# Kernel optimization log

Measured on AMD Instinct MI355X. Metric: run time of the kernel, lower is better.

Reference implementation:

```python
import jax, jax.numpy as jnp
import numpy as np
from jax import lax

B, N, C = 2, 4160, 512
HID = 2048
NUM_HEADS = 4
HEAD_DIM = C // NUM_HEADS
LN_EPS = 1e-5


def setup_inputs() -> dict:
    key = jax.random.key(0)
    ks = jax.random.split(key, 16)
    std = 0.02
    inp = {
        "x": jax.random.normal(ks[0], (B, N, C), dtype=jnp.float32),
        "ln1_w": jnp.ones((C,), jnp.float32), "ln1_b": jnp.zeros((C,), jnp.float32),
        "ln2_w": jnp.ones((C,), jnp.float32), "ln2_b": jnp.zeros((C,), jnp.float32),
        "q_w": jax.random.normal(ks[1], (C, C), jnp.float32) * std,
        "q_b": jnp.zeros((C,), jnp.float32),
        "kv_w": jax.random.normal(ks[2], (2 * C, C), jnp.float32) * std,
        "kv_b": jnp.zeros((2 * C,), jnp.float32),
        "proj_w": jax.random.normal(ks[3], (C, C), jnp.float32) * std,
        "proj_b": jnp.zeros((C,), jnp.float32),
        "fc1_w": jax.random.normal(ks[4], (HID, C), jnp.float32) * std,
        "fc1_b": jnp.zeros((HID,), jnp.float32),
        "dw_w": jax.random.normal(ks[5], (HID, 1, 3), jnp.float32) * np.sqrt(2.0 / 3.0),
        "dw_b": jnp.zeros((HID,), jnp.float32),
        "fc2_w": jax.random.normal(ks[6], (C, HID), jnp.float32) * std,
        "fc2_b": jnp.zeros((C,), jnp.float32),
        "px1_w": jax.random.normal(ks[7], (2 * C, C), jnp.float32) * std,
        "px1_b": jnp.zeros((2 * C,), jnp.float32),
        "px2_w": jax.random.normal(ks[8], (C, 2 * C), jnp.float32) * std,
        "px2_b": jnp.zeros((C,), jnp.float32),
        "gamma1": jnp.full((C,), 1e-6, jnp.float32),
        "gamma2": jnp.full((C,), 1e-6, jnp.float32),
        "H": 4096,
        "semantic_len": 64,
    }
    return inp


def _ln(x, w, b):
    mu = jnp.mean(x, axis=-1, keepdims=True)
    var = jnp.mean(jnp.square(x - mu), axis=-1, keepdims=True)
    return (x - mu) * lax.rsqrt(var + LN_EPS) * w + b


def _linear(x, w, b):
    return jnp.einsum('...i,oi->...o', x, w) + b


def _attention(x, q_w, q_b, kv_w, kv_b, proj_w, proj_b):
    b, n, c = x.shape
    h, d = NUM_HEADS, HEAD_DIM
    q = _linear(x, q_w, q_b).reshape(b, n, h, d).transpose(0, 2, 1, 3)   # bhnd
    kv = _linear(x, kv_w, kv_b).reshape(b, n, 2, h, d).transpose(2, 0, 3, 1, 4)
    k, v = kv[0], kv[1]                                                   # bhnd
    scale = d ** -0.5
    attn = jax.nn.softmax(jnp.einsum('bhnd,bhmd->bhnm', q, k) * scale, axis=-1)
    out = jnp.einsum('bhnm,bhmd->bhnd', attn, v).transpose(0, 2, 1, 3).reshape(b, n, c)
    return _linear(out, proj_w, proj_b)


def _dwconv(x, w, b):
    # x: [B, H, HID] -> conv over token axis, depthwise
    xt = x.transpose(0, 2, 1)  # NCH
    y = lax.conv_general_dilated(xt, w, window_strides=(1,), padding=((1, 1),),
                                 feature_group_count=HID,
                                 dimension_numbers=('NCH', 'OIH', 'NCH'))
    return (y + b[None, :, None]).transpose(0, 2, 1)


def _merge_ffn(x, H, fc1_w, fc1_b, dw_w, dw_b, fc2_w, fc2_b, px1_w, px1_b, px2_w, px2_b):
    seq = x[:, :H, :]
    sem = x[:, H:, :]
    sem = _linear(jax.nn.gelu(_linear(sem, px1_w, px1_b), approximate=False), px2_w, px2_b)
    seq = _linear(seq, fc1_w, fc1_b)
    seq = jax.nn.gelu(_dwconv(seq, dw_w, dw_b), approximate=False)
    seq = _linear(seq, fc2_w, fc2_b)
    return jnp.concatenate([seq, sem], axis=1)


def reference(x, ln1_w, ln1_b, ln2_w, ln2_b, q_w, q_b, kv_w, kv_b, proj_w, proj_b,
              fc1_w, fc1_b, dw_w, dw_b, fc2_w, fc2_b, px1_w, px1_b, px2_w, px2_b,
              gamma1, gamma2, H, semantic_len):
    x = x + gamma1 * _attention(_ln(x, ln1_w, ln1_b), q_w, q_b, kv_w, kv_b, proj_w, proj_b)
    x = x + gamma2 * _merge_ffn(_ln(x, ln2_w, ln2_b), H,
                                fc1_w, fc1_b, dw_w, dw_b, fc2_w, fc2_b,
                                px1_w, px1_b, px2_w, px2_b)
    return x
```

## Files before the change

### kernel.cpp

```cpp
#include <hip/hip_runtime.h>
#include <stdint.h>

#define BB 2
#define NN 4160
#define CC 512
#define HIDD 2048
#define HH 4096
#define QSCALE 0.12751742f
#define KSPLIT 6
#define KTILES 11

typedef short bf16x8 __attribute__((ext_vector_type(8)));
typedef float f32x4 __attribute__((ext_vector_type(4)));
typedef float f32x16 __attribute__((ext_vector_type(16)));

__device__ __forceinline__ float bf2f(ushort u){
  union { uint32_t u32; float f; } c; c.u32 = ((uint32_t)u) << 16; return c.f;
}
__device__ __forceinline__ ushort f2bf(float f){
  union { float f; uint32_t u32; } c; c.f = f;
  uint32_t r = c.u32 + 0x7fffu + ((c.u32 >> 16) & 1u);
  return (ushort)(r >> 16);
}
__device__ __forceinline__ float gelu_f(float x){
  return 0.5f * x * (1.0f + erff(x * 0.70710678118654752440f));
}
__device__ __forceinline__ void async16(ushort* lds, const ushort* g){
  __builtin_amdgcn_global_load_lds(
      (const __attribute__((address_space(1))) uint32_t*)g,
      (__attribute__((address_space(3))) uint32_t*)lds, 16, 0, 0);
}
__device__ __forceinline__ uint32_t cvtpk_bf16(float a, float b){
  uint32_t r;
  asm("v_cvt_pk_bf16_f32 %0, %1, %2" : "=v"(r) : "v"(a), "v"(b));
  return r;
}
__device__ __forceinline__ void swap32(uint32_t& x, uint32_t& y){
  asm("v_permlane32_swap_b32 %0, %1" : "+v"(x), "+v"(y));
}

template<int MODE>
__device__ __forceinline__ int rowmap(int m){
  if (MODE == 0) return m;
  if (MODE == 1) return (m >> 12) * NN + (m & 4095);
  return (m >> 6) * NN + HH + (m & 63);
}

__global__ __launch_bounds__(256) void wconv_kernel(
    const float* __restrict__ s0, const float* __restrict__ s1,
    const float* __restrict__ s2, const float* __restrict__ s3,
    const float* __restrict__ s4, const float* __restrict__ s5,
    const float* __restrict__ s6, ushort* __restrict__ dst)
{
  int i4 = (blockIdx.x * 256 + threadIdx.x) * 4;
  const float* s; int off;
  if      (i4 <  262144){ s = s0; off = 0;       }
  else if (i4 <  786432){ s = s1; off = 262144;  }
  else if (i4 < 1048576){ s = s2; off = 786432;  }
  else if (i4 < 2097152){ s = s3; off = 1048576; }
  else if (i4 < 3145728){ s = s4; off = 2097152; }
  else if (i4 < 3670016){ s = s5; off = 3145728; }
  else                  { s = s6; off = 3670016; }
  float4 v = *(const float4*)(s + (i4 - off));
  union { ushort h[4]; uint2 u; } o;
  o.h[0] = f2bf(v.x); o.h[1] = f2bf(v.y); o.h[2] = f2bf(v.z); o.h[3] = f2bf(v.w);
  *(uint2*)(dst + i4) = o.u;
}

__global__ __launch_bounds__(256) void ln_kernel(
    const float* __restrict__ x, const float* __restrict__ w,
    const float* __restrict__ b, ushort* __restrict__ out)
{
  int row  = blockIdx.x * 4 + (threadIdx.x >> 6);
  int lane = threadIdx.x & 63;
  const float4* xr = (const float4*)(x + (size_t)row * CC);
  float4 v0 = xr[lane];
  float4 v1 = xr[lane + 64];
  float s  = v0.x + v0.y + v0.z + v0.w + v1.x + v1.y + v1.z + v1.w;
  float ss = v0.x*v0.x + v0.y*v0.y + v0.z*v0.z + v0.w*v0.w
           + v1.x*v1.x + v1.y*v1.y + v1.z*v1.z + v1.w*v1.w;
  #pragma unroll
  for (int off = 1; off < 64; off <<= 1){
    s  += __shfl_xor(s, off);
    ss += __shfl_xor(ss, off);
  }
  float mu  = s * (1.0f / CC);
  float var = ss * (1.0f / CC) - mu * mu;
  float rs  = rsqrtf(var + 1e-5f);
  const float4* wp = (const float4*)w;
  const float4* bp = (const float4*)b;
  float4 w0 = wp[lane], w1 = wp[lane + 64], b0 = bp[lane], b1 = bp[lane + 64];
  union { ushort h[4]; uint2 u; } o0, o1;
  o0.h[0] = f2bf((v0.x - mu) * rs * w0.x + b0.x);
  o0.h[1] = f2bf((v0.y - mu) * rs * w0.y + b0.y);
  o0.h[2] = f2bf((v0.z - mu) * rs * w0.z + b0.z);
  o0.h[3] = f2bf((v0.w - mu) * rs * w0.w + b0.w);
  o1.h[0] = f2bf((v1.x - mu) * rs * w1.x + b1.x);
  o1.h[1] = f2bf((v1.y - mu) * rs * w1.y + b1.y);
  o1.h[2] = f2bf((v1.z - mu) * rs * w1.z + b1.z);
  o1.h[3] = f2bf((v1.w - mu) * rs * w1.w + b1.w);
  ushort* orow = out + (size_t)row * CC;
  ((uint2*)orow)[lane]      = o0.u;
  ((uint2*)orow)[lane + 64] = o1.u;
}

template<int BN, int AMAP, int OMAP, int EPI>
__global__ __launch_bounds__(256) void gemm_kernel(
    const ushort* __restrict__ A, int lda,
    const ushort* __restrict__ W,
    const float* __restrict__ bias, const float* __restrict__ bias2,
    ushort* __restrict__ outb, ushort* __restrict__ outb2,
    float* __restrict__ outf,
    const float* __restrict__ resid, const float* __restrict__ gamma,
    ushort* __restrict__ vt, int K, int O)
{
  constexpr int NCT = BN / 32;
  __shared__ __align__(16) ushort As[128 * 64];
  __shared__ __align__(16) ushort Ws[BN * 64];
  int tid  = threadIdx.x;
  int lane = tid & 63;
  int wv   = tid >> 6;
  int w0   = wv & 1, w1 = wv >> 1;
  int quad = lane >> 4, l16 = lane & 15;
  int m0 = blockIdx.x * 128;
  int o0 = blockIdx.y * BN;

  f32x4 acc[4][NCT];
  f32x4 zf = {0.f, 0.f, 0.f, 0.f};
  #pragma unroll
  for (int i = 0; i < 4; i++)
    #pragma unroll
    for (int j = 0; j < NCT; j++) acc[i][j] = zf;

  for (int k0 = 0; k0 < K; k0 += 64){
    __syncthreads();
    #pragma unroll
    for (int i = 0; i < 4; i++){
      int o = i * 256 + tid;
      int row = o >> 3, c = (o & 7) ^ (row & 7);
      int gm = rowmap<AMAP>(m0 + row);
      async16(&As[o * 8], A + (size_t)gm * lda + k0 + c * 8);
    }
    #pragma unroll
    for (int i = 0; i < BN * 8 / 256; i++){
      int o = i * 256 + tid;
      int row = o >> 3, c = (o & 7) ^ (row & 7);
      async16(&Ws[o * 8], W + (size_t)(o0 + row) * K + k0 + c * 8);
    }
    __syncthreads();
    #pragma unroll
    for (int kk = 0; kk < 2; kk++){
      bf16x8 af[4], bfr[NCT];
      #pragma unroll
      for (int rt = 0; rt < 4; rt++){
        int row = w1 * 64 + rt * 16 + l16;
        af[rt] = *(const bf16x8*)&As[(row * 8 + ((kk * 4 + quad) ^ (row & 7))) * 8];
      }
      #pragma unroll
      for (int ct = 0; ct < NCT; ct++){
        int row = w0 * (BN / 2) + ct * 16 + l16;
        bfr[ct] = *(const bf16x8*)&Ws[(row * 8 + ((kk * 4 + quad) ^ (row & 7))) * 8];
      }
      #pragma unroll
      for (int rt = 0; rt < 4; rt++)
        #pragma unroll
        for (int ct = 0; ct < NCT; ct++)
          acc[rt][ct] = __builtin_amdgcn_mfma_f32_16x16x32_bf16(af[rt], bfr[ct], acc[rt][ct], 0, 0, 0);
    }
  }

  #pragma unroll
  for (int ct = 0; ct < NCT; ct++){
    int col = o0 + w0 * (BN / 2) + ct * 16 + l16;
    #pragma unroll
    for (int rt = 0; rt < 4; rt++){
      int mb = m0 + w1 * 64 + rt * 16 + quad * 4;
      if (EPI == 3){
        if (col < 512){
          float bs = bias[col];
          #pragma unroll
          for (int r = 0; r < 4; r++)
            outb[(size_t)(mb + r) * 512 + col] = f2bf((acc[rt][ct][r] + bs) * QSCALE);
        } else if (col < 1024){
          float bs = bias2[col - 512];
          #pragma unroll
          for (int r = 0; r < 4; r++)
            outb2[(size_t)(mb + r) * 512 + (col - 512)] = f2bf(acc[rt][ct][r] + bs);
        } else {
          float bs = bias2[col - 512];
          int dd = col - 1024;
          int h2 = dd >> 7, d = dd & 127;
          int bbat = (mb >= NN) ? 1 : 0;
          int n = mb - bbat * NN;
          union { ushort h[4]; uint2 u; } pk;
          #pragma unroll
          for (int r = 0; r < 4; r++) pk.h[r] = f2bf(acc[rt][ct][r] + bs);
          *(uint2*)&vt[((size_t)((bbat * 4 + h2) * 128 + d)) * NN + n] = pk.u;
        }
      } else {
        float bs = bias[col];
        #pragma unroll
        for (int r = 0; r < 4; r++){
          float v = acc[rt][ct][r] + bs;
          if (EPI == 1) v = gelu_f(v);
          if (EPI == 0 || EPI == 1){
            outb[(size_t)rowmap<OMAP>(mb + r) * O + col] = f2bf(v);
          } else {
            size_t off = (size_t)rowmap<OMAP>(mb + r) * O + col;
            outf[off] = resid[off] + gamma[col] * v;
          }
        }
      }
    }
  }
}

__global__ __launch_bounds__(256, 2) void attn_kernel(
    const ushort* __restrict__ q, const ushort* __restrict__ kbuf,
    const ushort* __restrict__ vt, ushort* __restrict__ opart, float* __restrict__ ml)
{
  __shared__ __align__(16) ushort Ks[2][64 * 128];
  __shared__ __align__(16) ushort VTs[2][128 * 64];
  __shared__ float Als[4][32];
  int tid = threadIdx.x, lane = tid & 63, wv = tid >> 6;
  int l31 = lane & 31, hf = lane >> 5;
  int qt = blockIdx.x, bh = blockIdx.y, ks = blockIdx.z;
  int b = bh >> 2, h = bh & 3;
  int jt0 = ks * KTILES;
  int jt1 = jt0 + KTILES; if (jt1 > 65) jt1 = 65;

  const ushort* kg0 = kbuf + ((size_t)b * NN) * CC + h * 128;
  const ushort* vg0 = vt + ((size_t)bh * 128) * NN;

  auto stage = [&](int bsel, int t){
    const ushort* kgb = kg0 + (size_t)(t * 64) * CC;
    const ushort* vgb = vg0 + t * 64;
    #pragma unroll
    for (int i = 0; i < 4; i++){
      int oo = i * 256 + tid;
      int row = oo >> 4, ck = (oo & 15) ^ (row & 7);
      async16(&Ks[bsel][oo * 8], kgb + (size_t)row * CC + ck * 8);
      int d = oo >> 3, cv = (oo & 7) ^ (d & 7);
      async16(&VTs[bsel][oo * 8], vgb + (size_t)d * NN + cv * 8);
    }
  };

  stage(0, jt0);

  int qr = qt * 128 + wv * 32 + l31;
  qr = (qr < NN) ? qr : (NN - 1);
  const ushort* qrow = q + ((size_t)(b * NN + qr)) * CC + h * 128 + hf * 8;
  bf16x8 qf[8];
  #pragma unroll
  for (int kk = 0; kk < 8; kk++)
    qf[kk] = *(const bf16x8*)(qrow + kk * 16);

  float mrow = -1e30f, lrow = 0.f;
  f32x16 o[4];
  #pragma unroll
  for (int dt = 0; dt < 4; dt++)
    #pragma unroll
    for (int r = 0; r < 16; r++) o[dt][r] = 0.f;

  int cur = 0;
  for (int jt = jt0; jt < jt1; jt++){
    __syncthreads();
    if (jt + 1 < jt1) stage(cur ^ 1, jt + 1);
    const ushort* Kb = Ks[cur];
    const ushort* Vb = VTs[cur];

    f32x16 s0, s1;
    #pragma unroll
    for (int r = 0; r < 16; r++){ s0[r] = 0.f; s1[r] = 0.f; }
    __builtin_amdgcn_s_setprio(1);
    #pragma unroll
    for (int kk = 0; kk < 8; kk++){
      int r0 = l31, r1 = 32 + l31;
      bf16x8 kf0 = *(const bf16x8*)&Kb[(r0 * 16 + ((kk * 2 + hf) ^ (r0 & 7))) * 8];
      bf16x8 kf1 = *(const bf16x8*)&Kb[(r1 * 16 + ((kk * 2 + hf) ^ (r1 & 7))) * 8];
      s0 = __builtin_amdgcn_mfma_f32_32x32x16_bf16(kf0, qf[kk], s0, 0, 0, 0);
      s1 = __builtin_amdgcn_mfma_f32_32x32x16_bf16(kf1, qf[kk], s1, 0, 0, 0);
    }
    __builtin_amdgcn_s_setprio(0);

    float mx = s0[0];
    #pragma unroll
    for (int r = 1; r < 16; r++) mx = fmaxf(mx, s0[r]);
    #pragma unroll
    for (int r = 0; r < 16; r++) mx = fmaxf(mx, s1[r]);
    mx = fmaxf(mx, __shfl_xor(mx, 32));

    if (__any(mx > mrow + 8.0f)){
      float mn = fmaxf(mrow, mx);
      float al = __builtin_amdgcn_exp2f(mrow - mn);
      mrow = mn;
      lrow *= al;
      if (lane < 32) Als[wv][l31] = al;
      #pragma unroll
      for (int g = 0; g < 4; g++){
        float4 ag = *(const float4*)&Als[wv][8 * g + 4 * hf];
        float agr[4] = {ag.x, ag.y, ag.z, ag.w};
        #pragma unroll
        for (int dt = 0; dt < 4; dt++)
          #pragma unroll
          for (int r = 0; r < 4; r++)
            o[dt][4 * g + r] *= agr[r];
      }
    }

    float t = 0.f;
    #pragma unroll
    for (int r = 0; r < 16; r++){ s0[r] = __builtin_amdgcn_exp2f(s0[r] - mrow); t += s0[r]; }
    #pragma unroll
    for (int r = 0; r < 16; r++){ s1[r] = __builtin_amdgcn_exp2f(s1[r] - mrow); t += s1[r]; }
    t += __shfl_xor(t, 32);
    lrow += t;

    union PU { uint32_t w[4]; bf16x8 v; };
    bf16x8 pa[4];
    {
      uint32_t Aw = cvtpk_bf16(s0[0],  s0[1]);
      uint32_t Bw = cvtpk_bf16(s0[2],  s0[3]);
      uint32_t Cw = cvtpk_bf16(s0[4],  s0[5]);
      uint32_t Dw = cvtpk_bf16(s0[6],  s0[7]);
      swap32(Aw, Cw); swap32(Bw, Dw);
      PU u0; u0.w[0] = Aw; u0.w[1] = Bw; u0.w[2] = Cw; u0.w[3] = Dw; pa[0] = u0.v;
      uint32_t Ew = cvtpk_bf16(s0[8],  s0[9]);
      uint32_t Fw = cvtpk_bf16(s0[10], s0[11]);
      uint32_t Gw = cvtpk_bf16(s0[12], s0[13]);
      uint32_t Hw = cvtpk_bf16(s0[14], s0[15]);
      swap32(Ew, Gw); swap32(Fw, Hw);
      PU u1; u1.w[0] = Ew; u1.w[1] = Fw; u1.w[2] = Gw; u1.w[3] = Hw; pa[1] = u1.v;
      uint32_t Iw = cvtpk_bf16(s1[0],  s1[1]);
      uint32_t Jw = cvtpk_bf16(s1[2],  s1[3]);
      uint32_t Kw = cvtpk_bf16(s1[4],  s1[5]);
      uint32_t Lw = cvtpk_bf16(s1[6],  s1[7]);
      swap32(Iw, Kw); swap32(Jw, Lw);
      PU u2; u2.w[0] = Iw; u2.w[1] = Jw; u2.w[2] = Kw; u2.w[3] = Lw; pa[2] = u2.v;
      uint32_t Mw = cvtpk_bf16(s1[8],  s1[9]);
      uint32_t Nw = cvtpk_bf16(s1[10], s1[11]);
      uint32_t Ow = cvtpk_bf16(s1[12], s1[13]);
      uint32_t Pw = cvtpk_bf16(s1[14], s1[15]);
      swap32(Mw, Ow); swap32(Nw, Pw);
      PU u3; u3.w[0] = Mw; u3.w[1] = Nw; u3.w[2] = Ow; u3.w[3] = Pw; pa[3] = u3.v;
    }

    __builtin_amdgcn_s_setprio(1);
    #pragma unroll
    for (int k4 = 0; k4 < 4; k4++)
      #pragma unroll
      for (int dt = 0; dt < 4; dt++){
        int d = dt * 32 + l31;
        bf16x8 vf = *(const bf16x8*)&Vb[(d * 8 + ((k4 * 2 + hf) ^ (d & 7))) * 8];
        o[dt] = __builtin_amdgcn_mfma_f32_32x32x16_bf16(pa[k4], vf, o[dt], 0, 0, 0);
      }
    __builtin_amdgcn_s_setprio(0);
    cur ^= 1;
  }

  int part = (qt * 8 + bh) * KSPLIT + ks;
  if (lane < 32){
    ml[(size_t)part * 256 + wv * 32 + l31]       = mrow;
    ml[(size_t)part * 256 + 128 + wv * 32 + l31] = lrow;
  }
  ushort* op = opart + (size_t)part * 16384;
  #pragma unroll
  for (int g = 0; g < 4; g++)
    #pragma unroll
    for (int dt = 0; dt < 4; dt++){
      uint2 pk;
      pk.x = cvtpk_bf16(o[dt][4 * g + 0], o[dt][4 * g + 1]);
      pk.y = cvtpk_bf16(o[dt][4 * g + 2], o[dt][4 * g + 3]);
      *(uint2*)&op[((((wv * 4 + g) * 4 + dt) * 64) + lane) * 4] = pk;
    }
}

__global__ __launch_bounds__(256) void attn_combine_kernel(
    const ushort* __restrict__ opart, const float* __restrict__ ml,
    ushort* __restrict__ out)
{
  int qt = blockIdx.x, bh = blockIdx.y;
  int b = bh >> 2, hd = bh & 3;
  int tid = threadIdx.x, lane = tid & 63, wq = tid >> 6;
  int l31 = lane & 31, hf = lane >> 5;
  int base = (qt * 8 + bh) * KSPLIT;

  #pragma unroll
  for (int g = 0; g < 4; g++){
    int qb = wq * 32 + 8 * g + 4 * hf;
    float mv[KSPLIT][4], lv[KSPLIT][4];
    #pragma unroll
    for (int p = 0; p < KSPLIT; p++){
      float4 m = *(const float4*)&ml[(size_t)(base + p) * 256 + qb];
      float4 l = *(const float4*)&ml[(size_t)(base + p) * 256 + 128 + qb];
      mv[p][0] = m.x; mv[p][1] = m.y; mv[p][2] = m.z; mv[p][3] = m.w;
      lv[p][0] = l.x; lv[p][1] = l.y; lv[p][2] = l.z; lv[p][3] = l.w;
    }
    float wr[KSPLIT][4], invr[4];
    #pragma unroll
    for (int r = 0; r < 4; r++){
      float mx = mv[0][r];
      #pragma unroll
      for (int p = 1; p < KSPLIT; p++) mx = fmaxf(mx, mv[p][r]);
      float den = 0.f;
      #pragma unroll
      for (int p = 0; p < KSPLIT; p++){
        wr[p][r] = __builtin_amdgcn_exp2f(mv[p][r] - mx);
        den += wr[p][r] * lv[p][r];
      }
      invr[r] = 1.0f / den;
    }
    #pragma unroll
    for (int dt = 0; dt < 4; dt++){
      int idx = (((wq * 4 + g) * 4 + dt) * 64 + lane) * 4;
      float acc[4] = {0.f, 0.f, 0.f, 0.f};
      #pragma unroll
      for (int p = 0; p < KSPLIT; p++){
        union { ushort h[4]; uint2 u; } a;
        a.u = *(const uint2*)&opart[(size_t)(base + p) * 16384 + idx];
        #pragma unroll
        for (int r = 0; r < 4; r++) acc[r] += wr[p][r] * bf2f(a.h[r]);
      }
      #pragma unroll
      for (int r = 0; r < 4; r++){
        int n = qt * 128 + qb + r;
        if (n < NN)
          out[((size_t)(b * NN + n)) * CC + hd * 128 + dt * 32 + l31] = f2bf(acc[r] * invr[r]);
      }
    }
  }
}

__global__ __launch_bounds__(256) void dwconv_kernel(
    const ushort* __restrict__ u, const float* __restrict__ w,
    const float* __restrict__ bia, ushort* __restrict__ out)
{
  int g = blockIdx.x * 256 + threadIdx.x;
  int row = g >> 8;
  int c8 = (g & 255) * 8;
  int n = row & (HH - 1);
  size_t base = (size_t)row * HIDD + c8;
  uint4 z4; z4.x = z4.y = z4.z = z4.w = 0;
  uint4 u1 = *(const uint4*)(u + base);
  uint4 u0 = (n > 0)      ? *(const uint4*)(u + base - HIDD) : z4;
  uint4 u2 = (n < HH - 1) ? *(const uint4*)(u + base + HIDD) : z4;
  const ushort* p0 = (const ushort*)&u0;
  const ushort* p1 = (const ushort*)&u1;
  const ushort* p2 = (const ushort*)&u2;
  union { ushort h[8]; uint4 v; } o;
  #pragma unroll
  for (int k = 0; k < 8; k++){
    int c = c8 + k;
    float acc = bia[c] + w[c * 3] * bf2f(p0[k]) + w[c * 3 + 1] * bf2f(p1[k]) + w[c * 3 + 2] * bf2f(p2[k]);
    o.h[k] = f2bf(gelu_f(acc));
  }
  *(uint4*)(out + base) = o.v;
}

extern "C" void kernel_launch(void* const* d_in, const int* in_sizes, int n_in,
                              void* d_out, int out_size, void* d_ws, size_t ws_size,
                              hipStream_t stream)
{
  const float* x      = (const float*)d_in[0];
  const float* ln1w   = (const float*)d_in[1];
  const float* ln1b   = (const float*)d_in[2];
  const float* ln2w   = (const float*)d_in[3];
  const float* ln2b   = (const float*)d_in[4];
  const float* q_b    = (const float*)d_in[6];
  const float* kv_b   = (const float*)d_in[8];
  const float* proj_b = (const float*)d_in[10];
  const float* fc1_b  = (const float*)d_in[12];
  const float* dw_w   = (const float*)d_in[13];
  const float* dw_b   = (const float*)d_in[14];
  const float* fc2_b  = (const float*)d_in[16];
  const float* px1_b  = (const float*)d_in[18];
  const float* px2_b  = (const float*)d_in[20];
  const float* gamma1 = (const float*)d_in[21];
  const float* gamma2 = (const float*)d_in[22];
  float* out = (float*)d_out;

  char* ws = (char*)d_ws;
  ushort* wbf = (ushort*)(ws);
  ushort* lnb = (ushort*)(ws + 8388608);
  ushort* qb  = (ushort*)(ws + 16908288);
  ushort* kb  = (ushort*)(ws + 25427968);
  ushort* vtb = (ushort*)(ws + 33947648);
  ushort* ab  = (ushort*)(ws + 42467328);
  ushort* opart = (ushort*)(ws + 50987008);
  float*  mlb   = (float*)(ws + 102891520);
  ushort* f1  = (ushort*)(ws + 50987008);
  ushort* dg  = (ushort*)(ws + 84541440);
  ushort* sm1 = (ushort*)(ws + 118095872);

  ushort* wq    = wbf;
  ushort* wproj = wbf + 786432;
  ushort* wfc1  = wbf + 1048576;
  ushort* wfc2  = wbf + 2097152;
  ushort* wpx1  = wbf + 3145728;
  ushort* wpx2  = wbf + 3670016;

  wconv_kernel<<<4096, 256, 0, stream>>>((const float*)d_in[5], (const float*)d_in[7],
                                         (const float*)d_in[9], (const float*)d_in[11],
                                         (const float*)d_in[15], (const float*)d_in[17],
                                         (const float*)d_in[19], wbf);
  ln_kernel<<<2080, 256, 0, stream>>>(x, ln1w, ln1b, lnb);
  gemm_kernel<128,0,0,3><<<dim3(65, 12), 256, 0, stream>>>(
      lnb, 512, wq, q_b, kv_b, qb, kb, nullptr, nullptr, nullptr, vtb, 512, 1536);
  attn_kernel<<<dim3(33, 8, KSPLIT), 256, 0, stream>>>(qb, kb, vtb, opart, mlb);
  attn_combine_kernel<<<dim3(33, 8), 256, 0, stream>>>(opart, mlb, ab);
  gemm_kernel<64,0,0,2><<<dim3(65, 8), 256, 0, stream>>>(
      ab, 512, wproj, proj_b, nullptr, nullptr, nullptr, out, x, gamma1, nullptr, 512, 512);
  ln_kernel<<<2080, 256, 0, stream>>>(out, ln2w, ln2b, lnb);
  gemm_kernel<128,1,0,0><<<dim3(64, 16), 256, 0, stream>>>(
      lnb, 512, wfc1, fc1_b, nullptr, f1, nullptr, nullptr, nullptr, nullptr, nullptr, 512, 2048);
  dwconv_kernel<<<8192, 256, 0, stream>>>(f1, dw_w, dw_b, dg);
  gemm_kernel<64,0,1,2><<<dim3(64, 8), 256, 0, stream>>>(
      dg, 2048, wfc2, fc2_b, nullptr, nullptr, nullptr, out, out, gamma2, nullptr, 2048, 512);
  gemm_kernel<64,2,0,1><<<dim3(1, 16), 256, 0, stream>>>(
      lnb, 512, wpx1, px1_b, nullptr, sm1, nullptr, nullptr, nullptr, nullptr, nullptr, 512, 1024);
  gemm_kernel<64,0,2,2><<<dim3(1, 8), 256, 0, stream>>>(
      sm1, 1024, wpx2, px2_b, nullptr, nullptr, nullptr, out, out, gamma2, nullptr, 1024, 512);
}
```

Before: 461.4 us.

## Halve attention KV tile to 32 rows and raise occupancy to four blocks

```diff
diff --git a/kernel.cpp b/kernel.cpp
--- a/kernel.cpp
+++ b/kernel.cpp
@@ -7,8 +7,9 @@
 #define HIDD 2048
 #define HH 4096
 #define QSCALE 0.12751742f
-#define KSPLIT 6
-#define KTILES 11
+#define KSPLIT 7
+#define KTILES 19
+#define NKT 130
 
 typedef short bf16x8 __attribute__((ext_vector_type(8)));
 typedef float f32x4 __attribute__((ext_vector_type(4)));
@@ -215,32 +216,32 @@
   }
 }
 
-__global__ __launch_bounds__(256, 2) void attn_kernel(
+__global__ __launch_bounds__(256, 4) void attn_kernel(
     const ushort* __restrict__ q, const ushort* __restrict__ kbuf,
     const ushort* __restrict__ vt, ushort* __restrict__ opart, float* __restrict__ ml)
 {
-  __shared__ __align__(16) ushort Ks[2][64 * 128];
-  __shared__ __align__(16) ushort VTs[2][128 * 64];
+  __shared__ __align__(16) ushort Ks[2][32 * 128];
+  __shared__ __align__(16) ushort VTs[2][128 * 32];
   __shared__ float Als[4][32];
   int tid = threadIdx.x, lane = tid & 63, wv = tid >> 6;
   int l31 = lane & 31, hf = lane >> 5;
   int qt = blockIdx.x, bh = blockIdx.y, ks = blockIdx.z;
   int b = bh >> 2, h = bh & 3;
   int jt0 = ks * KTILES;
-  int jt1 = jt0 + KTILES; if (jt1 > 65) jt1 = 65;
+  int jt1 = jt0 + KTILES; if (jt1 > NKT) jt1 = NKT;
 
   const ushort* kg0 = kbuf + ((size_t)b * NN) * CC + h * 128;
   const ushort* vg0 = vt + ((size_t)bh * 128) * NN;
 
   auto stage = [&](int bsel, int t){
-    const ushort* kgb = kg0 + (size_t)(t * 64) * CC;
-    const ushort* vgb = vg0 + t * 64;
-    #pragma unroll
-    for (int i = 0; i < 4; i++){
+    const ushort* kgb = kg0 + (size_t)(t * 32) * CC;
+    const ushort* vgb = vg0 + t * 32;
+    #pragma unroll
+    for (int i = 0; i < 2; i++){
       int oo = i * 256 + tid;
       int row = oo >> 4, ck = (oo & 15) ^ (row & 7);
       async16(&Ks[bsel][oo * 8], kgb + (size_t)row * CC + ck * 8);
-      int d = oo >> 3, cv = (oo & 7) ^ (d & 7);
+      int d = oo >> 2, cv = (oo & 3) ^ (d & 3);
       async16(&VTs[bsel][oo * 8], vgb + (size_t)d * NN + cv * 8);
     }
   };
@@ -269,25 +270,23 @@
     const ushort* Kb = Ks[cur];
     const ushort* Vb = VTs[cur];
 
-    f32x16 s0, s1;
-    #pragma unroll
-    for (int r = 0; r < 16; r++){ s0[r] = 0.f; s1[r] = 0.f; }
+    f32x16 s0;
+    #pragma unroll
+    for (int r = 0; r < 16; r++) s0[r] = 0.f;
     __builtin_amdgcn_s_setprio(1);
     #pragma unroll
     for (int kk = 0; kk < 8; kk++){
-      int r0 = l31, r1 = 32 + l31;
+      int r0 = l31;
       bf16x8 kf0 = *(const bf16x8*)&Kb[(r0 * 16 + ((kk * 2 + hf) ^ (r0 & 7))) * 8];
-      bf16x8 kf1 = *(const bf16x8*)&Kb[(r1 * 16 + ((kk * 2 + hf) ^ (r1 & 7))) * 8];
       s0 = __builtin_amdgcn_mfma_f32_32x32x16_bf16(kf0, qf[kk], s0, 0, 0, 0);
-      s1 = __builtin_amdgcn_mfma_f32_32x32x16_bf16(kf1, qf[kk], s1, 0, 0, 0);
     }
     __builtin_amdgcn_s_setprio(0);
 
-    float mx = s0[0];
-    #pragma unroll
-    for (int r = 1; r < 16; r++) mx = fmaxf(mx, s0[r]);
-    #pragma unroll
-    for (int r = 0; r < 16; r++) mx = fmaxf(mx, s1[r]);
+    float mx = fmaxf(
+        fmaxf(fmaxf(fmaxf(s0[0], s0[1]),  fmaxf(s0[2],  s0[3])),
+              fmaxf(fmaxf(s0[4], s0[5]),  fmaxf(s0[6],  s0[7]))),
+        fmaxf(fmaxf(fmaxf(s0[8], s0[9]),  fmaxf(s0[10], s0[11])),
+              fmaxf(fmaxf(s0[12], s0[13]), fmaxf(s0[14], s0[15]))));
     mx = fmaxf(mx, __shfl_xor(mx, 32));
 
     if (__any(mx > mrow + 8.0f)){
@@ -308,21 +307,20 @@
       }
     }
 
-    float t = 0.f;
-    #pragma unroll
-    for (int r = 0; r < 16; r++){ s0[r] = __builtin_amdgcn_exp2f(s0[r] - mrow); t += s0[r]; }
-    #pragma unroll
-    for (int r = 0; r < 16; r++){ s1[r] = __builtin_amdgcn_exp2f(s1[r] - mrow); t += s1[r]; }
+    #pragma unroll
+    for (int r = 0; r < 16; r++) s0[r] = __builtin_amdgcn_exp2f(s0[r] - mrow);
+    float t = (((s0[0] + s0[1]) + (s0[2] + s0[3])) + ((s0[4] + s0[5]) + (s0[6] + s0[7])))
+            + (((s0[8] + s0[9]) + (s0[10] + s0[11])) + ((s0[12] + s0[13]) + (s0[14] + s0[15])));
     t += __shfl_xor(t, 32);
     lrow += t;
 
     union PU { uint32_t w[4]; bf16x8 v; };
-    bf16x8 pa[4];
+    bf16x8 pa[2];
     {
-      uint32_t Aw = cvtpk_bf16(s0[0],  s0[1]);
-      uint32_t Bw = cvtpk_bf16(s0[2],  s0[3]);
-      uint32_t Cw = cvtpk_bf16(s0[4],  s0[5]);
-      uint32_t Dw = cvtpk_bf16(s0[6],  s0[7]);
+      uint32_t Aw = cvtpk_bf16(s0[0], s0[1]);
+      uint32_t Bw = cvtpk_bf16(s0[2], s0[3]);
+      uint32_t Cw = cvtpk_bf16(s0[4], s0[5]);
+      uint32_t Dw = cvtpk_bf16(s0[6], s0[7]);
       swap32(Aw, Cw); swap32(Bw, Dw);
       PU u0; u0.w[0] = Aw; u0.w[1] = Bw; u0.w[2] = Cw; u0.w[3] = Dw; pa[0] = u0.v;
       uint32_t Ew = cvtpk_bf16(s0[8],  s0[9]);
@@ -331,27 +329,15 @@
       uint32_t Hw = cvtpk_bf16(s0[14], s0[15]);
       swap32(Ew, Gw); swap32(Fw, Hw);
       PU u1; u1.w[0] = Ew; u1.w[1] = Fw; u1.w[2] = Gw; u1.w[3] = Hw; pa[1] = u1.v;
-      uint32_t Iw = cvtpk_bf16(s1[0],  s1[1]);
-      uint32_t Jw = cvtpk_bf16(s1[2],  s1[3]);
-      uint32_t Kw = cvtpk_bf16(s1[4],  s1[5]);
-      uint32_t Lw = cvtpk_bf16(s1[6],  s1[7]);
-      swap32(Iw, Kw); swap32(Jw, Lw);
-      PU u2; u2.w[0] = Iw; u2.w[1] = Jw; u2.w[2] = Kw; u2.w[3] = Lw; pa[2] = u2.v;
-      uint32_t Mw = cvtpk_bf16(s1[8],  s1[9]);
-      uint32_t Nw = cvtpk_bf16(s1[10], s1[11]);
-      uint32_t Ow = cvtpk_bf16(s1[12], s1[13]);
-      uint32_t Pw = cvtpk_bf16(s1[14], s1[15]);
-      swap32(Mw, Ow); swap32(Nw, Pw);
-      PU u3; u3.w[0] = Mw; u3.w[1] = Nw; u3.w[2] = Ow; u3.w[3] = Pw; pa[3] = u3.v;
     }
 
     __builtin_amdgcn_s_setprio(1);
     #pragma unroll
-    for (int k4 = 0; k4 < 4; k4++)
+    for (int k4 = 0; k4 < 2; k4++)
       #pragma unroll
       for (int dt = 0; dt < 4; dt++){
         int d = dt * 32 + l31;
-        bf16x8 vf = *(const bf16x8*)&Vb[(d * 8 + ((k4 * 2 + hf) ^ (d & 7))) * 8];
+        bf16x8 vf = *(const bf16x8*)&Vb[(d * 4 + ((k4 * 2 + hf) ^ (d & 3))) * 8];
         o[dt] = __builtin_amdgcn_mfma_f32_32x32x16_bf16(pa[k4], vf, o[dt], 0, 0, 0);
       }
     __builtin_amdgcn_s_setprio(0);
@@ -487,7 +473,7 @@
   ushort* vtb = (ushort*)(ws + 33947648);
   ushort* ab  = (ushort*)(ws + 42467328);
   ushort* opart = (ushort*)(ws + 50987008);
-  float*  mlb   = (float*)(ws + 102891520);
+  float*  mlb   = (float*)(ws + 111542272);
   ushort* f1  = (ushort*)(ws + 50987008);
   ushort* dg  = (ushort*)(ws + 84541440);
   ushort* sm1 = (ushort*)(ws + 118095872);
```

Measured after the change: 580.3 us. +25.8%, slower.
